# Kernel tuning notes

Measured on AMD Instinct MI355X. Metric: run time of the kernel, lower is better.

## Reference

```python
import jax, jax.numpy as jnp
import numpy as np

K = 5           # kernel_size from kernel_kwargs
P = K // 2      # padding (same-size output)
MASK_TH = 0.5   # mask_th init kwarg
EPS = 1e-6

# squared distance of each of the K*K taps from the kernel center, shape [K*K]
_R2 = jnp.asarray(np.array([(dy - P) ** 2 + (dx - P) ** 2
                            for dy in range(K) for dx in range(K)], dtype=np.float32))


def setup_inputs() -> dict:
    key = jax.random.key(0)
    k1, k2 = jax.random.split(key)
    bev_map = jax.random.normal(k1, (4, 1, 768, 768), dtype=jnp.float32)
    # per-pixel scales in [0.5, 2.0) -- realistic kernel bandwidths
    bev_scale = 0.5 + 1.5 * jax.random.uniform(k2, (4, 1, 768, 768), dtype=jnp.float32)
    return {"bev_map": bev_map, "bev_scale": bev_scale}


def reference(bev_map, bev_scale):
    B, C, H, W = bev_map.shape
    x = jax.nn.relu(bev_map)                                   # non_neg = ReLU
    xp = jnp.pad(x, ((0, 0), (0, 0), (P, P), (P, P)))
    # unfold: [B, C, K*K, H, W] shifted views of the padded map
    patches = jnp.stack([xp[:, :, dy:dy + H, dx:dx + W]
                         for dy in range(K) for dx in range(K)], axis=2)
    # ScaleAdaptiveExpKernel: Gaussian weights from per-pixel scale
    # w: [B, 1, K*K, H, W]
    w = jnp.exp(-_R2[None, None, :, None, None]
                / (2.0 * jnp.square(bev_scale)[:, :, None] + EPS))
    bev_map_conv = jnp.sum(patches * w, axis=2)                # [B, C, H, W]
    mask = (bev_map_conv >= MASK_TH).astype(bev_map_conv.dtype)
    return bev_map_conv, mask
```

## Files before the change

### kernel.cpp

```cpp
#include <hip/hip_runtime.h>

#define HH 768
#define WW 768
#define BC 4
#define NPIX (BC * HH * WW)

typedef float f4 __attribute__((ext_vector_type(4)));
typedef float f2 __attribute__((ext_vector_type(2)));

__global__ __launch_bounds__(256) void conv_thresh_kernel(
    const float* __restrict__ bev_map,
    const float* __restrict__ bev_scale,
    float* __restrict__ out)
{
    const int tx = threadIdx.x;
    const int ty = threadIdx.y;
    const int x0 = (blockIdx.x * 64 + tx) * 4;
    const int y0 = blockIdx.y * 8 + ty * 2;
    const int b  = blockIdx.z;

    const size_t plane = (size_t)b * (HH * WW);
    const float* __restrict__ m = bev_map + plane;

    float h0[6][4], h1[6][4], h2[6][4];

#pragma unroll
    for (int r = 0; r < 6; ++r) {
        const int yy = y0 - 2 + r;
        const bool yok = (unsigned)yy < (unsigned)HH;
        const float* rowp = m + yy * WW + x0;
        f4 t;
        if (yok) {
            t = *(const f4*)rowp;
            t.x = fmaxf(t.x, 0.f); t.y = fmaxf(t.y, 0.f);
            t.z = fmaxf(t.z, 0.f); t.w = fmaxf(t.w, 0.f);
        } else {
            t.x = 0.f; t.y = 0.f; t.z = 0.f; t.w = 0.f;
        }
        float lz = __shfl_up(t.z, 1);
        float lw = __shfl_up(t.w, 1);
        float rx = __shfl_down(t.x, 1);
        float ry = __shfl_down(t.y, 1);
        if (tx == 0) {
            lz = 0.f; lw = 0.f;
            if (yok && x0 != 0) {
                f2 t2 = *(const f2*)(rowp - 2);
                lz = fmaxf(t2.x, 0.f); lw = fmaxf(t2.y, 0.f);
            }
        }
        if (tx == 63) {
            rx = 0.f; ry = 0.f;
            if (yok && x0 != WW - 4) {
                f2 t2 = *(const f2*)(rowp + 4);
                rx = fmaxf(t2.x, 0.f); ry = fmaxf(t2.y, 0.f);
            }
        }
        const float w0 = lz, w1 = lw, w2 = t.x, w3 = t.y,
                    w4 = t.z, w5 = t.w, w6 = rx, w7 = ry;
        h0[r][0] = w2; h1[r][0] = w1 + w3; h2[r][0] = w0 + w4;
        h0[r][1] = w3; h1[r][1] = w2 + w4; h2[r][1] = w1 + w5;
        h0[r][2] = w4; h1[r][2] = w3 + w5; h2[r][2] = w2 + w6;
        h0[r][3] = w5; h1[r][3] = w4 + w6; h2[r][3] = w3 + w7;
    }

#pragma unroll
    for (int k = 0; k < 2; ++k) {
        const int oy = y0 + k;
        const size_t idx = plane + (size_t)oy * WW + x0;
        const f4 scv = *(const f4*)(bev_scale + idx);
        f4 conv, mask;
#pragma unroll
        for (int j = 0; j < 4; ++j) {
            const float c0 = h0[k + 2][j];
            const float s1 = h1[k + 2][j] + h0[k + 1][j] + h0[k + 3][j];
            const float s2 = h1[k + 1][j] + h1[k + 3][j];
            const float s4 = h2[k + 2][j] + h0[k][j]     + h0[k + 4][j];
            const float s5 = h2[k + 1][j] + h2[k + 3][j] + h1[k][j] + h1[k + 4][j];
            const float s8 = h2[k][j]     + h2[k + 4][j];

            const float sc = scv[j];
            const float t1 = -1.0f / (2.0f * sc * sc + 1e-6f);
            const float e1 = __expf(t1);
            const float e2 = e1 * e1;
            const float e4 = e2 * e2;
            const float e5 = e4 * e1;
            const float e8 = e4 * e4;

            float cv = c0;
            cv = fmaf(e1, s1, cv);
            cv = fmaf(e2, s2, cv);
            cv = fmaf(e4, s4, cv);
            cv = fmaf(e5, s5, cv);
            cv = fmaf(e8, s8, cv);
            conv[j] = cv;
            mask[j] = (cv >= 0.5f) ? 1.0f : 0.0f;
        }
        *(f4*)(out + idx) = conv;
        *(f4*)(out + idx + (size_t)NPIX) = mask;
    }
}

extern "C" void kernel_launch(void* const* d_in, const int* in_sizes, int n_in,
                              void* d_out, int out_size, void* d_ws, size_t ws_size,
                              hipStream_t stream) {
    const float* bev_map   = (const float*)d_in[0];
    const float* bev_scale = (const float*)d_in[1];
    float* out = (float*)d_out;

    dim3 block(64, 4, 1);
    dim3 grid(WW / 256, HH / 8, BC);
    conv_thresh_kernel<<<grid, block, 0, stream>>>(bev_map, bev_scale, out);
}
```

Before: 76.68 us.

## Compute one output row per thread with streaming row accumulation

```diff
diff --git a/kernel.cpp b/kernel.cpp
--- a/kernel.cpp
+++ b/kernel.cpp
@@ -8,7 +8,7 @@
 typedef float f4 __attribute__((ext_vector_type(4)));
 typedef float f2 __attribute__((ext_vector_type(2)));
 
-__global__ __launch_bounds__(256) void conv_thresh_kernel(
+__global__ __launch_bounds__(256, 8) void conv_thresh_kernel(
     const float* __restrict__ bev_map,
     const float* __restrict__ bev_scale,
     float* __restrict__ out)
@@ -16,17 +16,25 @@
     const int tx = threadIdx.x;
     const int ty = threadIdx.y;
     const int x0 = (blockIdx.x * 64 + tx) * 4;
-    const int y0 = blockIdx.y * 8 + ty * 2;
+    const int oy = blockIdx.y * 4 + ty;
     const int b  = blockIdx.z;
 
     const size_t plane = (size_t)b * (HH * WW);
     const float* __restrict__ m = bev_map + plane;
+    const size_t idx = plane + (size_t)oy * WW + x0;
 
-    float h0[6][4], h1[6][4], h2[6][4];
+    const f4 scv = *(const f4*)(bev_scale + idx);
+
+    float c0[4], s1[4], s2[4], s4[4], s5[4], s8[4];
+#pragma unroll
+    for (int j = 0; j < 4; ++j) {
+        c0[j] = 0.f; s1[j] = 0.f; s2[j] = 0.f;
+        s4[j] = 0.f; s5[j] = 0.f; s8[j] = 0.f;
+    }
 
 #pragma unroll
-    for (int r = 0; r < 6; ++r) {
-        const int yy = y0 - 2 + r;
+    for (int r = 0; r < 5; ++r) {
+        const int yy = oy - 2 + r;
         const bool yok = (unsigned)yy < (unsigned)HH;
         const float* rowp = m + yy * WW + x0;
         f4 t;
@@ -57,47 +65,43 @@
         }
         const float w0 = lz, w1 = lw, w2 = t.x, w3 = t.y,
                     w4 = t.z, w5 = t.w, w6 = rx, w7 = ry;
-        h0[r][0] = w2; h1[r][0] = w1 + w3; h2[r][0] = w0 + w4;
-        h0[r][1] = w3; h1[r][1] = w2 + w4; h2[r][1] = w1 + w5;
-        h0[r][2] = w4; h1[r][2] = w3 + w5; h2[r][2] = w2 + w6;
-        h0[r][3] = w5; h1[r][3] = w4 + w6; h2[r][3] = w3 + w7;
+        const float h0[4] = { w2, w3, w4, w5 };
+        const float h1[4] = { w1 + w3, w2 + w4, w3 + w5, w4 + w6 };
+        const float h2[4] = { w0 + w4, w1 + w5, w2 + w6, w3 + w7 };
+        if (r == 0 || r == 4) {
+#pragma unroll
+            for (int j = 0; j < 4; ++j) { s4[j] += h0[j]; s5[j] += h1[j]; s8[j] += h2[j]; }
+        } else if (r == 1 || r == 3) {
+#pragma unroll
+            for (int j = 0; j < 4; ++j) { s1[j] += h0[j]; s2[j] += h1[j]; s5[j] += h2[j]; }
+        } else {
+#pragma unroll
+            for (int j = 0; j < 4; ++j) { c0[j] = h0[j]; s1[j] += h1[j]; s4[j] += h2[j]; }
+        }
     }
 
+    f4 conv, mask;
 #pragma unroll
-    for (int k = 0; k < 2; ++k) {
-        const int oy = y0 + k;
-        const size_t idx = plane + (size_t)oy * WW + x0;
-        const f4 scv = *(const f4*)(bev_scale + idx);
-        f4 conv, mask;
-#pragma unroll
-        for (int j = 0; j < 4; ++j) {
-            const float c0 = h0[k + 2][j];
-            const float s1 = h1[k + 2][j] + h0[k + 1][j] + h0[k + 3][j];
-            const float s2 = h1[k + 1][j] + h1[k + 3][j];
-            const float s4 = h2[k + 2][j] + h0[k][j]     + h0[k + 4][j];
-            const float s5 = h2[k + 1][j] + h2[k + 3][j] + h1[k][j] + h1[k + 4][j];
-            const float s8 = h2[k][j]     + h2[k + 4][j];
-
-            const float sc = scv[j];
-            const float t1 = -1.0f / (2.0f * sc * sc + 1e-6f);
-            const float e1 = __expf(t1);
-            const float e2 = e1 * e1;
-            const float e4 = e2 * e2;
-            const float e5 = e4 * e1;
-            const float e8 = e4 * e4;
-
-            float cv = c0;
-            cv = fmaf(e1, s1, cv);
-            cv = fmaf(e2, s2, cv);
-            cv = fmaf(e4, s4, cv);
-            cv = fmaf(e5, s5, cv);
-            cv = fmaf(e8, s8, cv);
-            conv[j] = cv;
-            mask[j] = (cv >= 0.5f) ? 1.0f : 0.0f;
-        }
-        *(f4*)(out + idx) = conv;
-        *(f4*)(out + idx + (size_t)NPIX) = mask;
+    for (int j = 0; j < 4; ++j) {
+        const float sc  = scv[j];
+        const float den = fmaf(2.0f * sc, sc, 1e-6f);
+        const float t1  = -__builtin_amdgcn_rcpf(den);
+        const float e1  = __expf(t1);
+        const float e2  = e1 * e1;
+        const float e4  = e2 * e2;
+        const float e5  = e4 * e1;
+        const float e8  = e4 * e4;
+        float cv = c0[j];
+        cv = fmaf(e1, s1[j], cv);
+        cv = fmaf(e2, s2[j], cv);
+        cv = fmaf(e4, s4[j], cv);
+        cv = fmaf(e5, s5[j], cv);
+        cv = fmaf(e8, s8[j], cv);
+        conv[j] = cv;
+        mask[j] = (cv >= 0.5f) ? 1.0f : 0.0f;
     }
+    *(f4*)(out + idx) = conv;
+    *(f4*)(out + idx + (size_t)NPIX) = mask;
 }
 
 extern "C" void kernel_launch(void* const* d_in, const int* in_sizes, int n_in,
@@ -108,6 +112,6 @@
     float* out = (float*)d_out;
 
     dim3 block(64, 4, 1);
-    dim3 grid(WW / 256, HH / 8, BC);
+    dim3 grid(WW / 256, HH / 4, BC);
     conv_thresh_kernel<<<grid, block, 0, stream>>>(bev_map, bev_scale, out);
 }
```

After: 81.41 us. 6.2% more time.

## Hoist all loads up front, replace shuffles with halo loads, use fast reciprocal

Applied to the files above, without the earlier changes.

```diff
diff --git a/kernel.cpp b/kernel.cpp
--- a/kernel.cpp
+++ b/kernel.cpp
@@ -22,41 +22,48 @@
     const size_t plane = (size_t)b * (HH * WW);
     const float* __restrict__ m = bev_map + plane;
 
-    float h0[6][4], h1[6][4], h2[6][4];
+    const bool okL = (x0 != 0);
+    const bool okR = (x0 != WW - 4);
 
+    const size_t idx0 = plane + (size_t)y0 * WW + x0;
+    const f4 sc0v = *(const f4*)(bev_scale + idx0);
+    const f4 sc1v = *(const f4*)(bev_scale + idx0 + WW);
+
+    f4 A[6];
+    f2 L[6];
+    f2 R[6];
+    float ym[6];
 #pragma unroll
     for (int r = 0; r < 6; ++r) {
-        const int yy = y0 - 2 + r;
-        const bool yok = (unsigned)yy < (unsigned)HH;
-        const float* rowp = m + yy * WW + x0;
-        f4 t;
-        if (yok) {
-            t = *(const f4*)rowp;
-            t.x = fmaxf(t.x, 0.f); t.y = fmaxf(t.y, 0.f);
-            t.z = fmaxf(t.z, 0.f); t.w = fmaxf(t.w, 0.f);
-        } else {
-            t.x = 0.f; t.y = 0.f; t.z = 0.f; t.w = 0.f;
-        }
-        float lz = __shfl_up(t.z, 1);
-        float lw = __shfl_up(t.w, 1);
-        float rx = __shfl_down(t.x, 1);
-        float ry = __shfl_down(t.y, 1);
-        if (tx == 0) {
-            lz = 0.f; lw = 0.f;
-            if (yok && x0 != 0) {
-                f2 t2 = *(const f2*)(rowp - 2);
-                lz = fmaxf(t2.x, 0.f); lw = fmaxf(t2.y, 0.f);
-            }
-        }
-        if (tx == 63) {
-            rx = 0.f; ry = 0.f;
-            if (yok && x0 != WW - 4) {
-                f2 t2 = *(const f2*)(rowp + 4);
-                rx = fmaxf(t2.x, 0.f); ry = fmaxf(t2.y, 0.f);
-            }
-        }
-        const float w0 = lz, w1 = lw, w2 = t.x, w3 = t.y,
-                    w4 = t.z, w5 = t.w, w6 = rx, w7 = ry;
+        const int yy  = y0 - 2 + r;
+        const int yyc = yy < 0 ? 0 : (yy > HH - 1 ? HH - 1 : yy);
+        ym[r] = ((unsigned)yy < (unsigned)HH) ? 1.0f : 0.0f;
+        const float* rowp = m + yyc * WW + x0;
+        A[r] = *(const f4*)rowp;
+        L[r] = *(const f2*)(okL ? rowp - 2 : rowp);
+        R[r] = *(const f2*)(okR ? rowp + 4 : rowp);
+    }
+
+    float h0[6][4], h1[6][4], h2[6][4];
+#pragma unroll
+    for (int r = 0; r < 6; ++r) {
+        const float mr = ym[r];
+        float w0 = okL ? L[r].x : 0.f;
+        float w1 = okL ? L[r].y : 0.f;
+        float w2 = A[r].x;
+        float w3 = A[r].y;
+        float w4 = A[r].z;
+        float w5 = A[r].w;
+        float w6 = okR ? R[r].x : 0.f;
+        float w7 = okR ? R[r].y : 0.f;
+        w0 = fmaxf(w0, 0.f) * mr;
+        w1 = fmaxf(w1, 0.f) * mr;
+        w2 = fmaxf(w2, 0.f) * mr;
+        w3 = fmaxf(w3, 0.f) * mr;
+        w4 = fmaxf(w4, 0.f) * mr;
+        w5 = fmaxf(w5, 0.f) * mr;
+        w6 = fmaxf(w6, 0.f) * mr;
+        w7 = fmaxf(w7, 0.f) * mr;
         h0[r][0] = w2; h1[r][0] = w1 + w3; h2[r][0] = w0 + w4;
         h0[r][1] = w3; h1[r][1] = w2 + w4; h2[r][1] = w1 + w5;
         h0[r][2] = w4; h1[r][2] = w3 + w5; h2[r][2] = w2 + w6;
@@ -67,7 +74,7 @@
     for (int k = 0; k < 2; ++k) {
         const int oy = y0 + k;
         const size_t idx = plane + (size_t)oy * WW + x0;
-        const f4 scv = *(const f4*)(bev_scale + idx);
+        const f4 scv = (k == 0) ? sc0v : sc1v;
         f4 conv, mask;
 #pragma unroll
         for (int j = 0; j < 4; ++j) {
@@ -78,13 +85,14 @@
             const float s5 = h2[k + 1][j] + h2[k + 3][j] + h1[k][j] + h1[k + 4][j];
             const float s8 = h2[k][j]     + h2[k + 4][j];
 
-            const float sc = scv[j];
-            const float t1 = -1.0f / (2.0f * sc * sc + 1e-6f);
-            const float e1 = __expf(t1);
-            const float e2 = e1 * e1;
-            const float e4 = e2 * e2;
-            const float e5 = e4 * e1;
-            const float e8 = e4 * e4;
+            const float sc  = scv[j];
+            const float den = fmaf(2.0f * sc, sc, 1e-6f);
+            const float t1  = -__builtin_amdgcn_rcpf(den);
+            const float e1  = __expf(t1);
+            const float e2  = e1 * e1;
+            const float e4  = e2 * e2;
+            const float e5  = e4 * e1;
+            const float e8  = e4 * e4;
 
             float cv = c0;
             cv = fmaf(e1, s1, cv);
```

Result: faster. 74.41 us (-3.0%).
